# Kernel tuning notes

Measured on AMD Instinct MI355X. Metric: run time of the kernel, lower is better.

The kernel has to match this reference:

```python
import jax, jax.numpy as jnp
import numpy as np
from jax import lax

N = 4096      # network_size
B = 1024      # batch
AVG_DEG = 6.0 # scale-free preferential attachment adds ~3 edges/node (undirected)
N_STEPS = 10


def setup_inputs() -> dict:
    key = jax.random.key(0)
    k_in, k_adj = jax.random.split(key)
    external_input = jax.random.normal(k_in, (B, N), dtype=jnp.float32)
    # symmetric binary adjacency with average degree ~6 (stand-in for scale-free topology)
    a = jax.random.bernoulli(k_adj, AVG_DEG / N, (N, N))
    connectivity = jnp.maximum(a, a.T).astype(jnp.float32)
    connectivity = connectivity * (1.0 - jnp.eye(N, dtype=jnp.float32))  # no self-loops
    membrane_potentials = jnp.zeros((N,), dtype=jnp.float32)  # nn.Parameter init zeros
    thresholds = jnp.ones((N,), dtype=jnp.float32)            # nn.Parameter init ones
    refractory_periods = jnp.zeros((N,), dtype=jnp.float32)   # nn.Parameter init zeros
    return {
        "external_input": external_input,
        "connectivity": connectivity,
        "membrane_potentials": membrane_potentials,
        "thresholds": thresholds,
        "refractory_periods": refractory_periods,
    }


def reference(external_input, connectivity, membrane_potentials, thresholds, refractory_periods):
    b, n = external_input.shape
    v0 = membrane_potentials[None, :] + external_input          # [B, N]
    s0 = jnp.zeros((b, n), dtype=external_input.dtype)          # spikes

    def step(carry, _):
        v, s, refr = carry
        v = v + 0.1 * (s @ connectivity)                         # network input
        mask = (v > thresholds[None, :]) & (refr == 0.0)[None, :]
        new_s = mask.astype(v.dtype)
        v = jnp.where(mask, 0.0, v)                              # reset on spike
        refr = jnp.where(jnp.any(mask, axis=0), 3.0, refr)       # set refractory
        refr = jnp.clip(refr - 1.0, 0.0, 10.0)                   # decay
        v = v * 0.95                                             # leak
        return (v, new_s, refr), None

    (_, spikes, _), _ = lax.scan(step, (v0, s0, refractory_periods), None, length=N_STEPS)
    return spikes
```

## Files before the change

kernel.cpp:

```cpp
#include <hip/hip_runtime.h>
#include <stdint.h>

#define N_ 4096
#define B_ 1024
#define ROWB 512
#define NSTEPS_ 10
#define DEG_SLOTS 40
#define PAD_E ((uint32_t)(N_ * ROWB))
#define NBLK 256
#define NCTR 16
#define FLAGI 512

#define OFF_BAR  0
#define OFF_DEG  8192
#define OFF_NBR  24576
#define OFF_SEXP 679936
#define SEXP_BUF ((N_ + 1) * ROWB)

__global__ __launch_bounds__(256) void build_k(const float* __restrict__ C,
                                               uint32_t* __restrict__ deg,
                                               uint32_t* __restrict__ nbr,
                                               uint32_t* __restrict__ bar,
                                               uint32_t* __restrict__ pad0,
                                               uint32_t* __restrict__ pad1) {
    __shared__ uint32_t cnt;
    int tid = threadIdx.x;
    int n = blockIdx.x;
    if (n == 0) { for (int i = tid; i < 1056; i += 256) bar[i] = 0u; }
    else if (n == 1) { if (tid < 128) pad0[tid] = 0u; }
    else if (n == 2) { if (tid < 128) pad1[tid] = 0u; }
    if (tid == 0) cnt = 0;
    __syncthreads();
    const float4* row = (const float4*)(C + (size_t)n * N_);
    for (int j4 = tid; j4 < N_ / 4; j4 += 256) {
        float4 v = row[j4];
        int base = j4 * 4;
        #pragma unroll
        for (int q = 0; q < 4; ++q) {
            float f = (q == 0) ? v.x : (q == 1) ? v.y : (q == 2) ? v.z : v.w;
            if (f != 0.0f) {
                uint32_t p = atomicAdd(&cnt, 1u);
                uint32_t m = (uint32_t)(base + q);
                if (p < DEG_SLOTS) nbr[n * DEG_SLOTS + p] = m * (uint32_t)ROWB;
            }
        }
    }
    __syncthreads();
    uint32_t c = min(cnt, (uint32_t)DEG_SLOTS);
    if (tid == 0) deg[n] = c;
    if (tid < DEG_SLOTS && (uint32_t)tid >= c)
        nbr[n * DEG_SLOTS + tid] = PAD_E;
}

__device__ __forceinline__ void gbar(uint32_t* bar, uint32_t phase) {
    __syncthreads();
    int tid = threadIdx.x, bid = blockIdx.x;
    if (tid == 0)
        __hip_atomic_fetch_add(&bar[(bid & (NCTR - 1)) * 32], 1u,
                               __ATOMIC_RELAXED, __HIP_MEMORY_SCOPE_AGENT);
    if (bid == 0) {
        if (tid < NCTR) {
            uint32_t tgt = (NBLK / NCTR) * phase;
            while (__hip_atomic_load(&bar[tid * 32], __ATOMIC_RELAXED,
                                     __HIP_MEMORY_SCOPE_AGENT) < tgt)
                __builtin_amdgcn_s_sleep(1);
        }
        __syncthreads();
        if (tid == 0)
            __hip_atomic_store(&bar[FLAGI], phase,
                               __ATOMIC_RELAXED, __HIP_MEMORY_SCOPE_AGENT);
    }
    if (tid == 0) {
        while (__hip_atomic_load(&bar[FLAGI], __ATOMIC_RELAXED,
                                 __HIP_MEMORY_SCOPE_AGENT) < phase)
            __builtin_amdgcn_s_sleep(1);
        (void)__hip_atomic_load(&bar[FLAGI], __ATOMIC_ACQUIRE,
                                __HIP_MEMORY_SCOPE_AGENT);
    }
    __syncthreads();
}

__global__ __launch_bounds__(1024, 4) void persist_k(const float* __restrict__ ext,
                                                     const float* __restrict__ memb,
                                                     const float* __restrict__ thr,
                                                     const float* __restrict__ refr_in,
                                                     const uint32_t* __restrict__ deg,
                                                     const uint32_t* __restrict__ nbr,
                                                     unsigned char* __restrict__ sExp,
                                                     float* __restrict__ out,
                                                     uint32_t* bar) {
    __shared__ uint32_t s_nbr[16 * DEG_SLOTS];
    __shared__ unsigned char bt[16][528];

    int bid = blockIdx.x;
    int n0 = bid * 16;
    int tid = threadIdx.x;
    int wv = tid >> 6, lane = tid & 63;
    int n = n0 + wv;
    int bbatch = lane * 16;
    int bbn = lane * 8;

    if (tid < 16 * DEG_SLOTS) s_nbr[tid] = nbr[(size_t)n0 * DEG_SLOTS + tid];
    __syncthreads();

    float tn = thr[n];
    float r  = refr_in[n];
    uint32_t dg = __builtin_amdgcn_readfirstlane(deg[n]);
    const uint32_t* lst = &s_nbr[wv * DEG_SLOTS];

    float v[16];
    {
        float mb = memb[n];
        #pragma unroll
        for (int i = 0; i < 16; ++i)
            v[i] = __fadd_rn(mb, ext[(size_t)(bbatch + i) * N_ + n]);
    }

    uint32_t nib0 = 0, nib1 = 0;

    {
        uint32_t nb = (r != 0.0f) ? 0u : 1u;
        #pragma unroll
        for (int i = 0; i < 16; ++i) {
            int sp = (v[i] > tn) && nb;
            if (i < 8) nib0 |= (uint32_t)sp << (4 * i);
            else       nib1 |= (uint32_t)sp << (4 * (i - 8));
            v[i] = __fmul_rn(sp ? 0.0f : v[i], 0.95f);
        }
        unsigned long long p0 = (unsigned long long)nib0 | ((unsigned long long)nib1 << 32);
        __hip_atomic_store((unsigned long long*)(sExp + (size_t)n * ROWB + bbn), p0,
                           __ATOMIC_RELAXED, __HIP_MEMORY_SCOPE_AGENT);
        int any = (__ballot((nib0 | nib1) != 0) != 0ull);
        r = any ? 3.0f : r;
        r = fminf(fmaxf(__fadd_rn(r, -1.0f), 0.0f), 10.0f);
    }
    gbar(bar, 1);

    unsigned char* sprev = sExp;
    unsigned char* snext = sExp + (size_t)SEXP_BUF;
    for (int s = 1; s < NSTEPS_; ++s) {
        uint32_t nb = (r != 0.0f) ? 0u : 1u;
        uint2 accA = make_uint2(0u, 0u), accB = make_uint2(0u, 0u);
        uint2 accC = make_uint2(0u, 0u), accD = make_uint2(0u, 0u);
        #pragma unroll
        for (int j = 0; j < 8; ++j) {
            uint32_t e = lst[j];
            uint2 d2 = *(const uint2*)(sprev + e + bbn);
            accA.x += d2.x; accA.y += d2.y;
        }
        if (dg > 8) {
            #pragma unroll
            for (int j = 8; j < 16; ++j) {
                uint32_t e = lst[j];
                uint2 d2 = *(const uint2*)(sprev + e + bbn);
                accB.x += d2.x; accB.y += d2.y;
            }
        }
        if (dg > 16) {
            #pragma unroll
            for (int j = 16; j < 31; ++j) {
                uint32_t e = lst[j];
                uint2 d2 = *(const uint2*)(sprev + e + bbn);
                accC.x += d2.x; accC.y += d2.y;
            }
        }
        if (dg > 31) {
            #pragma unroll
            for (int j = 31; j < 40; ++j) {
                uint32_t e = lst[j];
                uint2 d2 = *(const uint2*)(sprev + e + bbn);
                accD.x += d2.x; accD.y += d2.y;
            }
        }
        uint32_t newn0 = 0, newn1 = 0;
        #pragma unroll
        for (int h = 0; h < 2; ++h) {
            uint32_t a = h ? accA.y : accA.x;
            uint32_t b = h ? accB.y : accB.x;
            uint32_t c = h ? accC.y : accC.x;
            uint32_t d = h ? accD.y : accD.x;
            uint32_t sumE = (a & 0x0F0F0F0Fu) + (b & 0x0F0F0F0Fu) +
                            (c & 0x0F0F0F0Fu) + (d & 0x0F0F0F0Fu);
            uint32_t sumO = ((a >> 4) & 0x0F0F0F0Fu) + ((b >> 4) & 0x0F0F0F0Fu) +
                            ((c >> 4) & 0x0F0F0F0Fu) + ((d >> 4) & 0x0F0F0F0Fu);
            uint32_t nh = 0;
            #pragma unroll
            for (int k = 0; k < 4; ++k) {
                float ce = (float)((sumE >> (8 * k)) & 255u);
                float co = (float)((sumO >> (8 * k)) & 255u);
                int be = h * 8 + 2 * k, bo = be + 1;
                float ve = __fadd_rn(v[be], __fmul_rn(0.1f, ce));
                float vo = __fadd_rn(v[bo], __fmul_rn(0.1f, co));
                int se = (ve > tn) && nb;
                int so = (vo > tn) && nb;
                nh |= (uint32_t)se << (4 * (2 * k));
                nh |= (uint32_t)so << (4 * (2 * k + 1));
                if (s < NSTEPS_ - 1) {
                    v[be] = __fmul_rn(se ? 0.0f : ve, 0.95f);
                    v[bo] = __fmul_rn(so ? 0.0f : vo, 0.95f);
                }
            }
            if (h == 0) newn0 = nh; else newn1 = nh;
        }
        nib0 = newn0; nib1 = newn1;
        if (s < NSTEPS_ - 1) {
            unsigned long long p0 = (unsigned long long)nib0 | ((unsigned long long)nib1 << 32);
            __hip_atomic_store((unsigned long long*)(snext + (size_t)n * ROWB + bbn), p0,
                               __ATOMIC_RELAXED, __HIP_MEMORY_SCOPE_AGENT);
            int any = (__ballot((nib0 | nib1) != 0) != 0ull);
            r = any ? 3.0f : r;
            r = fminf(fmaxf(__fadd_rn(r, -1.0f), 0.0f), 10.0f);
            gbar(bar, (uint32_t)s + 1);
        }
        unsigned char* t = sprev; sprev = snext; snext = t;
    }

    *(uint2*)&bt[wv][bbn] = make_uint2(nib0, nib1);
    __syncthreads();
    #pragma unroll
    for (int p = 0; p < 4; ++p) {
        int i = tid + p * 1024;
        int rrow = i >> 2, c4 = (i & 3) * 4;
        uint32_t shl = (uint32_t)(rrow & 1) * 4u;
        int col = rrow >> 1;
        float4 o;
        o.x = (float)((bt[c4 + 0][col] >> shl) & 1u);
        o.y = (float)((bt[c4 + 1][col] >> shl) & 1u);
        o.z = (float)((bt[c4 + 2][col] >> shl) & 1u);
        o.w = (float)((bt[c4 + 3][col] >> shl) & 1u);
        *(float4*)&out[(size_t)rrow * N_ + n0 + c4] = o;
    }
}

extern "C" void kernel_launch(void* const* d_in, const int* in_sizes, int n_in,
                              void* d_out, int out_size, void* d_ws, size_t ws_size,
                              hipStream_t stream) {
    const float* ext     = (const float*)d_in[0];
    const float* C       = (const float*)d_in[1];
    const float* memb    = (const float*)d_in[2];
    const float* thr     = (const float*)d_in[3];
    const float* refr_in = (const float*)d_in[4];

    char* ws = (char*)d_ws;
    uint32_t* bar    = (uint32_t*)(ws + OFF_BAR);
    uint32_t* deg    = (uint32_t*)(ws + OFF_DEG);
    uint32_t* nbr    = (uint32_t*)(ws + OFF_NBR);
    unsigned char* sExp = (unsigned char*)(ws + OFF_SEXP);
    float*    out    = (float*)d_out;

    build_k<<<dim3(N_), dim3(256), 0, stream>>>(
        C, deg, nbr, bar,
        (uint32_t*)(sExp + (size_t)N_ * ROWB),
        (uint32_t*)(sExp + (size_t)SEXP_BUF + (size_t)N_ * ROWB));

    void* args[] = {(void*)&ext, (void*)&memb, (void*)&thr, (void*)&refr_in,
                    (void*)&deg, (void*)&nbr, (void*)&sExp, (void*)&out,
                    (void*)&bar};
    hipLaunchCooperativeKernel((const void*)persist_k, dim3(NBLK), dim3(1024),
                               args, 0, stream);
}
```

Baseline: 128.1 us.

## Partition persistent kernel by batch, keep spike state in LDS

After: 252.1 us. +96.7%, slower.

```diff
diff --git a/kernel.cpp b/kernel.cpp
--- a/kernel.cpp
+++ b/kernel.cpp
@@ -3,32 +3,30 @@
 
 #define N_ 4096
 #define B_ 1024
-#define ROWB 512
+#define BPB 4
 #define NSTEPS_ 10
 #define DEG_SLOTS 40
-#define PAD_E ((uint32_t)(N_ * ROWB))
+#define PAD_E ((uint32_t)(N_ * 2))
 #define NBLK 256
 #define NCTR 16
 #define FLAGI 512
 
-#define OFF_BAR  0
-#define OFF_DEG  8192
-#define OFF_NBR  24576
-#define OFF_SEXP 679936
-#define SEXP_BUF ((N_ + 1) * ROWB)
+#define OFF_BAR    0
+#define OFF_COLANY 4224
+#define OFF_DEG    8832
+#define OFF_NBRT   25216
+
+__global__ void initbar_k(uint32_t* __restrict__ bar, uint32_t* __restrict__ colAny) {
+    for (int i = threadIdx.x; i < 1056; i += 256) bar[i] = 0u;
+    for (int i = threadIdx.x; i < 9 * 128; i += 256) colAny[i] = 0u;
+}
 
 __global__ __launch_bounds__(256) void build_k(const float* __restrict__ C,
                                                uint32_t* __restrict__ deg,
-                                               uint32_t* __restrict__ nbr,
-                                               uint32_t* __restrict__ bar,
-                                               uint32_t* __restrict__ pad0,
-                                               uint32_t* __restrict__ pad1) {
+                                               uint32_t* __restrict__ nbrT) {
     __shared__ uint32_t cnt;
     int tid = threadIdx.x;
     int n = blockIdx.x;
-    if (n == 0) { for (int i = tid; i < 1056; i += 256) bar[i] = 0u; }
-    else if (n == 1) { if (tid < 128) pad0[tid] = 0u; }
-    else if (n == 2) { if (tid < 128) pad1[tid] = 0u; }
     if (tid == 0) cnt = 0;
     __syncthreads();
     const float4* row = (const float4*)(C + (size_t)n * N_);
@@ -41,7 +39,7 @@
             if (f != 0.0f) {
                 uint32_t p = atomicAdd(&cnt, 1u);
                 uint32_t m = (uint32_t)(base + q);
-                if (p < DEG_SLOTS) nbr[n * DEG_SLOTS + p] = m * (uint32_t)ROWB;
+                if (p < DEG_SLOTS) nbrT[(size_t)p * N_ + n] = m * 2u;
             }
         }
     }
@@ -49,7 +47,7 @@
     uint32_t c = min(cnt, (uint32_t)DEG_SLOTS);
     if (tid == 0) deg[n] = c;
     if (tid < DEG_SLOTS && (uint32_t)tid >= c)
-        nbr[n * DEG_SLOTS + tid] = PAD_E;
+        nbrT[(size_t)tid * N_ + n] = PAD_E;
 }
 
 __device__ __forceinline__ void gbar(uint32_t* bar, uint32_t phase) {
@@ -85,150 +83,179 @@
                                                      const float* __restrict__ thr,
                                                      const float* __restrict__ refr_in,
                                                      const uint32_t* __restrict__ deg,
-                                                     const uint32_t* __restrict__ nbr,
-                                                     unsigned char* __restrict__ sExp,
+                                                     const uint32_t* __restrict__ nbrT,
+                                                     uint32_t* __restrict__ colAny,
                                                      float* __restrict__ out,
                                                      uint32_t* bar) {
-    __shared__ uint32_t s_nbr[16 * DEG_SLOTS];
-    __shared__ unsigned char bt[16][528];
-
-    int bid = blockIdx.x;
-    int n0 = bid * 16;
-    int tid = threadIdx.x;
-    int wv = tid >> 6, lane = tid & 63;
-    int n = n0 + wv;
-    int bbatch = lane * 16;
-    int bbn = lane * 8;
-
-    if (tid < 16 * DEG_SLOTS) s_nbr[tid] = nbr[(size_t)n0 * DEG_SLOTS + tid];
-    __syncthreads();
-
-    float tn = thr[n];
-    float r  = refr_in[n];
-    uint32_t dg = __builtin_amdgcn_readfirstlane(deg[n]);
-    const uint32_t* lst = &s_nbr[wv * DEG_SLOTS];
-
-    float v[16];
+    __shared__ uint16_t sp[2][4104];
+    __shared__ uint32_t anyLDS[128];
+
+    int bid = blockIdx.x, t = threadIdx.x;
+    int n4 = t * 4, b0 = bid * BPB;
+    if (t == 0) { sp[0][4096] = 0; sp[1][4096] = 0; }
+    if (t < 128) anyLDS[t] = 0u;
+
+    uint4 dg4 = *(const uint4*)&deg[n4];
+    uint32_t maxd = max(max(dg4.x, dg4.y), max(dg4.z, dg4.w));
+    float4 mb4 = *(const float4*)&memb[n4];
+    float4 th4 = *(const float4*)&thr[n4];
+    float4 rf4 = *(const float4*)&refr_in[n4];
+    float tn[4] = {th4.x, th4.y, th4.z, th4.w};
+    float r[4]  = {rf4.x, rf4.y, rf4.z, rf4.w};
+
+    float v[4][4];
+    #pragma unroll
+    for (int i = 0; i < 4; ++i) {
+        float4 e4 = *(const float4*)&ext[(size_t)(b0 + i) * N_ + n4];
+        v[0][i] = __fadd_rn(mb4.x, e4.x);
+        v[1][i] = __fadd_rn(mb4.y, e4.y);
+        v[2][i] = __fadd_rn(mb4.z, e4.z);
+        v[3][i] = __fadd_rn(mb4.w, e4.w);
+    }
+
+    uint32_t nib[4];
+
     {
-        float mb = memb[n];
-        #pragma unroll
-        for (int i = 0; i < 16; ++i)
-            v[i] = __fadd_rn(mb, ext[(size_t)(bbatch + i) * N_ + n]);
-    }
-
-    uint32_t nib0 = 0, nib1 = 0;
-
-    {
-        uint32_t nb = (r != 0.0f) ? 0u : 1u;
-        #pragma unroll
-        for (int i = 0; i < 16; ++i) {
-            int sp = (v[i] > tn) && nb;
-            if (i < 8) nib0 |= (uint32_t)sp << (4 * i);
-            else       nib1 |= (uint32_t)sp << (4 * (i - 8));
-            v[i] = __fmul_rn(sp ? 0.0f : v[i], 0.95f);
-        }
-        unsigned long long p0 = (unsigned long long)nib0 | ((unsigned long long)nib1 << 32);
-        __hip_atomic_store((unsigned long long*)(sExp + (size_t)n * ROWB + bbn), p0,
-                           __ATOMIC_RELAXED, __HIP_MEMORY_SCOPE_AGENT);
-        int any = (__ballot((nib0 | nib1) != 0) != 0ull);
-        r = any ? 3.0f : r;
-        r = fminf(fmaxf(__fadd_rn(r, -1.0f), 0.0f), 10.0f);
-    }
-    gbar(bar, 1);
-
-    unsigned char* sprev = sExp;
-    unsigned char* snext = sExp + (size_t)SEXP_BUF;
+        #pragma unroll
+        for (int k = 0; k < 4; ++k) {
+            uint32_t nbk = (r[k] != 0.0f) ? 0u : 1u;
+            uint32_t nn = 0;
+            #pragma unroll
+            for (int i = 0; i < 4; ++i) {
+                int spk = (v[k][i] > tn[k]) && nbk;
+                nn |= (uint32_t)spk << (4 * i);
+                v[k][i] = __fmul_rn(spk ? 0.0f : v[k][i], 0.95f);
+            }
+            nib[k] = nn;
+        }
+        unsigned long long pk = (unsigned long long)(nib[0] | (nib[1] << 16)) |
+                                ((unsigned long long)(nib[2] | (nib[3] << 16)) << 32);
+        *(unsigned long long*)&sp[0][n4] = pk;
+        uint32_t lnib = (((nib[0] != 0) ? 1u : 0u) | ((nib[1] != 0) ? 2u : 0u) |
+                         ((nib[2] != 0) ? 4u : 0u) | ((nib[3] != 0) ? 8u : 0u))
+                        << (4 * (t & 7));
+        __syncthreads();
+        if (lnib) atomicOr(&anyLDS[t >> 3], lnib);
+        __syncthreads();
+        if (t < 128) {
+            uint32_t a = anyLDS[t];
+            if (a) atomicOr(&colAny[t], a);
+            anyLDS[t] = 0u;
+        }
+        gbar(bar, 1);
+        uint32_t aw = colAny[t >> 3];
+        #pragma unroll
+        for (int k = 0; k < 4; ++k) {
+            int any = (aw >> (4 * (t & 7) + k)) & 1;
+            r[k] = any ? 3.0f : r[k];
+            r[k] = fminf(fmaxf(__fadd_rn(r[k], -1.0f), 0.0f), 10.0f);
+        }
+    }
+
+    int cur = 0;
     for (int s = 1; s < NSTEPS_; ++s) {
-        uint32_t nb = (r != 0.0f) ? 0u : 1u;
-        uint2 accA = make_uint2(0u, 0u), accB = make_uint2(0u, 0u);
-        uint2 accC = make_uint2(0u, 0u), accD = make_uint2(0u, 0u);
+        const char* spc = (const char*)sp[cur];
+        uint32_t A[4] = {0,0,0,0}, Bc[4] = {0,0,0,0};
+        uint32_t Cc[4] = {0,0,0,0}, Dc[4] = {0,0,0,0};
         #pragma unroll
         for (int j = 0; j < 8; ++j) {
-            uint32_t e = lst[j];
-            uint2 d2 = *(const uint2*)(sprev + e + bbn);
-            accA.x += d2.x; accA.y += d2.y;
-        }
-        if (dg > 8) {
+            uint4 e = *(const uint4*)&nbrT[(size_t)j * N_ + n4];
+            A[0] += *(const uint16_t*)(spc + e.x);
+            A[1] += *(const uint16_t*)(spc + e.y);
+            A[2] += *(const uint16_t*)(spc + e.z);
+            A[3] += *(const uint16_t*)(spc + e.w);
+        }
+        if (maxd > 8) {
             #pragma unroll
             for (int j = 8; j < 16; ++j) {
-                uint32_t e = lst[j];
-                uint2 d2 = *(const uint2*)(sprev + e + bbn);
-                accB.x += d2.x; accB.y += d2.y;
-            }
-        }
-        if (dg > 16) {
+                uint4 e = *(const uint4*)&nbrT[(size_t)j * N_ + n4];
+                Bc[0] += *(const uint16_t*)(spc + e.x);
+                Bc[1] += *(const uint16_t*)(spc + e.y);
+                Bc[2] += *(const uint16_t*)(spc + e.z);
+                Bc[3] += *(const uint16_t*)(spc + e.w);
+            }
+        }
+        if (maxd > 16) {
             #pragma unroll
             for (int j = 16; j < 31; ++j) {
-                uint32_t e = lst[j];
-                uint2 d2 = *(const uint2*)(sprev + e + bbn);
-                accC.x += d2.x; accC.y += d2.y;
-            }
-        }
-        if (dg > 31) {
+                uint4 e = *(const uint4*)&nbrT[(size_t)j * N_ + n4];
+                Cc[0] += *(const uint16_t*)(spc + e.x);
+                Cc[1] += *(const uint16_t*)(spc + e.y);
+                Cc[2] += *(const uint16_t*)(spc + e.z);
+                Cc[3] += *(const uint16_t*)(spc + e.w);
+            }
+        }
+        if (maxd > 31) {
             #pragma unroll
             for (int j = 31; j < 40; ++j) {
-                uint32_t e = lst[j];
-                uint2 d2 = *(const uint2*)(sprev + e + bbn);
-                accD.x += d2.x; accD.y += d2.y;
-            }
-        }
-        uint32_t newn0 = 0, newn1 = 0;
-        #pragma unroll
-        for (int h = 0; h < 2; ++h) {
-            uint32_t a = h ? accA.y : accA.x;
-            uint32_t b = h ? accB.y : accB.x;
-            uint32_t c = h ? accC.y : accC.x;
-            uint32_t d = h ? accD.y : accD.x;
-            uint32_t sumE = (a & 0x0F0F0F0Fu) + (b & 0x0F0F0F0Fu) +
-                            (c & 0x0F0F0F0Fu) + (d & 0x0F0F0F0Fu);
-            uint32_t sumO = ((a >> 4) & 0x0F0F0F0Fu) + ((b >> 4) & 0x0F0F0F0Fu) +
-                            ((c >> 4) & 0x0F0F0F0Fu) + ((d >> 4) & 0x0F0F0F0Fu);
-            uint32_t nh = 0;
+                uint4 e = *(const uint4*)&nbrT[(size_t)j * N_ + n4];
+                Dc[0] += *(const uint16_t*)(spc + e.x);
+                Dc[1] += *(const uint16_t*)(spc + e.y);
+                Dc[2] += *(const uint16_t*)(spc + e.z);
+                Dc[3] += *(const uint16_t*)(spc + e.w);
+            }
+        }
+        #pragma unroll
+        for (int k = 0; k < 4; ++k) {
+            uint32_t nbk = (r[k] != 0.0f) ? 0u : 1u;
+            uint32_t sumE = (A[k] & 0x0F0Fu) + (Bc[k] & 0x0F0Fu) +
+                            (Cc[k] & 0x0F0Fu) + (Dc[k] & 0x0F0Fu);
+            uint32_t sumO = ((A[k] >> 4) & 0x0F0Fu) + ((Bc[k] >> 4) & 0x0F0Fu) +
+                            ((Cc[k] >> 4) & 0x0F0Fu) + ((Dc[k] >> 4) & 0x0F0Fu);
+            float c0 = (float)(sumE & 255u), c2 = (float)(sumE >> 8);
+            float c1 = (float)(sumO & 255u), c3 = (float)(sumO >> 8);
+            float v0 = __fadd_rn(v[k][0], __fmul_rn(0.1f, c0));
+            float v1 = __fadd_rn(v[k][1], __fmul_rn(0.1f, c1));
+            float v2 = __fadd_rn(v[k][2], __fmul_rn(0.1f, c2));
+            float v3 = __fadd_rn(v[k][3], __fmul_rn(0.1f, c3));
+            int s0 = (v0 > tn[k]) && nbk;
+            int s1 = (v1 > tn[k]) && nbk;
+            int s2 = (v2 > tn[k]) && nbk;
+            int s3 = (v3 > tn[k]) && nbk;
+            nib[k] = (uint32_t)s0 | ((uint32_t)s1 << 4) |
+                     ((uint32_t)s2 << 8) | ((uint32_t)s3 << 12);
+            if (s < NSTEPS_ - 1) {
+                v[k][0] = __fmul_rn(s0 ? 0.0f : v0, 0.95f);
+                v[k][1] = __fmul_rn(s1 ? 0.0f : v1, 0.95f);
+                v[k][2] = __fmul_rn(s2 ? 0.0f : v2, 0.95f);
+                v[k][3] = __fmul_rn(s3 ? 0.0f : v3, 0.95f);
+            }
+        }
+        if (s < NSTEPS_ - 1) {
+            unsigned long long pk = (unsigned long long)(nib[0] | (nib[1] << 16)) |
+                                    ((unsigned long long)(nib[2] | (nib[3] << 16)) << 32);
+            *(unsigned long long*)&sp[cur ^ 1][n4] = pk;
+            uint32_t lnib = (((nib[0] != 0) ? 1u : 0u) | ((nib[1] != 0) ? 2u : 0u) |
+                             ((nib[2] != 0) ? 4u : 0u) | ((nib[3] != 0) ? 8u : 0u))
+                            << (4 * (t & 7));
+            __syncthreads();
+            if (lnib) atomicOr(&anyLDS[t >> 3], lnib);
+            __syncthreads();
+            if (t < 128) {
+                uint32_t a = anyLDS[t];
+                if (a) atomicOr(&colAny[s * 128 + t], a);
+                anyLDS[t] = 0u;
+            }
+            gbar(bar, (uint32_t)s + 1);
+            uint32_t aw = colAny[s * 128 + (t >> 3)];
             #pragma unroll
             for (int k = 0; k < 4; ++k) {
-                float ce = (float)((sumE >> (8 * k)) & 255u);
-                float co = (float)((sumO >> (8 * k)) & 255u);
-                int be = h * 8 + 2 * k, bo = be + 1;
-                float ve = __fadd_rn(v[be], __fmul_rn(0.1f, ce));
-                float vo = __fadd_rn(v[bo], __fmul_rn(0.1f, co));
-                int se = (ve > tn) && nb;
-                int so = (vo > tn) && nb;
-                nh |= (uint32_t)se << (4 * (2 * k));
-                nh |= (uint32_t)so << (4 * (2 * k + 1));
-                if (s < NSTEPS_ - 1) {
-                    v[be] = __fmul_rn(se ? 0.0f : ve, 0.95f);
-                    v[bo] = __fmul_rn(so ? 0.0f : vo, 0.95f);
-                }
-            }
-            if (h == 0) newn0 = nh; else newn1 = nh;
-        }
-        nib0 = newn0; nib1 = newn1;
-        if (s < NSTEPS_ - 1) {
-            unsigned long long p0 = (unsigned long long)nib0 | ((unsigned long long)nib1 << 32);
-            __hip_atomic_store((unsigned long long*)(snext + (size_t)n * ROWB + bbn), p0,
-                               __ATOMIC_RELAXED, __HIP_MEMORY_SCOPE_AGENT);
-            int any = (__ballot((nib0 | nib1) != 0) != 0ull);
-            r = any ? 3.0f : r;
-            r = fminf(fmaxf(__fadd_rn(r, -1.0f), 0.0f), 10.0f);
-            gbar(bar, (uint32_t)s + 1);
-        }
-        unsigned char* t = sprev; sprev = snext; snext = t;
-    }
-
-    *(uint2*)&bt[wv][bbn] = make_uint2(nib0, nib1);
-    __syncthreads();
+                int any = (aw >> (4 * (t & 7) + k)) & 1;
+                r[k] = any ? 3.0f : r[k];
+                r[k] = fminf(fmaxf(__fadd_rn(r[k], -1.0f), 0.0f), 10.0f);
+            }
+        }
+        cur ^= 1;
+    }
+
     #pragma unroll
-    for (int p = 0; p < 4; ++p) {
-        int i = tid + p * 1024;
-        int rrow = i >> 2, c4 = (i & 3) * 4;
-        uint32_t shl = (uint32_t)(rrow & 1) * 4u;
-        int col = rrow >> 1;
+    for (int i = 0; i < 4; ++i) {
         float4 o;
-        o.x = (float)((bt[c4 + 0][col] >> shl) & 1u);
-        o.y = (float)((bt[c4 + 1][col] >> shl) & 1u);
-        o.z = (float)((bt[c4 + 2][col] >> shl) & 1u);
-        o.w = (float)((bt[c4 + 3][col] >> shl) & 1u);
-        *(float4*)&out[(size_t)rrow * N_ + n0 + c4] = o;
+        o.x = (float)((nib[0] >> (4 * i)) & 1u);
+        o.y = (float)((nib[1] >> (4 * i)) & 1u);
+        o.z = (float)((nib[2] >> (4 * i)) & 1u);
+        o.w = (float)((nib[3] >> (4 * i)) & 1u);
+        *(float4*)&out[(size_t)(b0 + i) * N_ + n4] = o;
     }
 }
 
@@ -243,18 +270,16 @@
 
     char* ws = (char*)d_ws;
     uint32_t* bar    = (uint32_t*)(ws + OFF_BAR);
+    uint32_t* colAny = (uint32_t*)(ws + OFF_COLANY);
     uint32_t* deg    = (uint32_t*)(ws + OFF_DEG);
-    uint32_t* nbr    = (uint32_t*)(ws + OFF_NBR);
-    unsigned char* sExp = (unsigned char*)(ws + OFF_SEXP);
+    uint32_t* nbrT   = (uint32_t*)(ws + OFF_NBRT);
     float*    out    = (float*)d_out;
 
-    build_k<<<dim3(N_), dim3(256), 0, stream>>>(
-        C, deg, nbr, bar,
-        (uint32_t*)(sExp + (size_t)N_ * ROWB),
-        (uint32_t*)(sExp + (size_t)SEXP_BUF + (size_t)N_ * ROWB));
+    initbar_k<<<dim3(1), dim3(256), 0, stream>>>(bar, colAny);
+    build_k<<<dim3(N_), dim3(256), 0, stream>>>(C, deg, nbrT);
 
     void* args[] = {(void*)&ext, (void*)&memb, (void*)&thr, (void*)&refr_in,
-                    (void*)&deg, (void*)&nbr, (void*)&sExp, (void*)&out,
+                    (void*)&deg, (void*)&nbrT, (void*)&colAny, (void*)&out,
                     (void*)&bar};
     hipLaunchCooperativeKernel((const void*)persist_k, dim3(NBLK), dim3(1024),
                                args, 0, stream);
```
